# Kernel optimization log

Hardware: AMD Instinct MI355X
Metric: run time of the kernel (lower is better)

The kernel has to match this reference:

```python
import jax, jax.numpy as jnp
import numpy as np

T = 2_000_000  # seq_len
I, H, O = 2, 30, 1  # input_size, hidden_size, output_size


def setup_inputs() -> dict:
    key = jax.random.key(0)
    ks = jax.random.split(key, 7)
    s = 1.0 / np.sqrt(H)  # torch default uniform(-1/sqrt(H), 1/sqrt(H)) scale
    return {
        "x": jax.random.normal(ks[0], (T, I), dtype=jnp.float32),
        "W_ih": jax.random.uniform(ks[1], (H, I), jnp.float32, -s, s),
        "W_hh": jax.random.uniform(ks[2], (H, H), jnp.float32, -s, s),
        "b_ih": jax.random.uniform(ks[3], (H,), jnp.float32, -s, s),
        "b_hh": jax.random.uniform(ks[4], (H,), jnp.float32, -s, s),
        "W_fc": jax.random.uniform(ks[5], (O, H), jnp.float32, -s, s),
        "b_fc": jax.random.uniform(ks[6], (O,), jnp.float32, -s, s),
    }


def reference(x, W_ih, W_hh, b_ih, b_hh, W_fc, b_fc):
    # Elman RNN (torch.nn.RNN, tanh): h_t = tanh(x_t W_ih^T + b_ih + h_{t-1} W_hh^T + b_hh)
    # Precompute the input projection for all timesteps in one GEMM.
    xp = x @ W_ih.T + (b_ih + b_hh)  # [T, H]

    def step(h, xt):
        h = jnp.tanh(xt + h @ W_hh.T)
        return h, h

    h0 = jnp.zeros((H,), dtype=x.dtype)
    _, hs = jax.lax.scan(step, h0, xp)  # hs: [T, H]
    return hs @ W_fc.T + b_fc  # [T, O]
```

## Files before the change

kernel.cpp:

```cpp
#include <hip/hip_runtime.h>


#define T_LEN     2000000
#define HID       30
#define CHUNK_LEN 64
#define BURN      15
#define NBLOCK    512
#define WSTEPS    8
#define NWIN      10
#define NCHUNK_ST 31250

typedef __attribute__((ext_vector_type(8))) _Float16 half8;
typedef __attribute__((ext_vector_type(2))) __fp16   fp16x2;
typedef __attribute__((ext_vector_type(4))) float    float4v;

union h8u { half8 v8; fp16x2 v2[4]; unsigned u2[4]; };
union h2u { fp16x2 v; unsigned u; };

#define PREFETCH(O) {                                                        \
    _Pragma("unroll")                                                        \
    for (int s = 0; s < WSTEPS; ++s) {                                       \
        int tt = wbase + (O) * WSTEPS + s;                                   \
        tt = tt < 0 ? 0 : (tt >= T_LEN ? T_LEN - 1 : tt);                    \
        nxt[s] = xf2[tt];                                                    \
    }                                                                        \
}

#define CONVERT() {                                                          \
    _Pragma("unroll")                                                        \
    for (int s = 0; s < WSTEPS; ++s) {                                       \
        h2u c; c.v = __builtin_amdgcn_cvt_pkrtz(nxt[s].x, nxt[s].y);         \
        xcur[s] = c.u;                                                       \
    }                                                                        \
}

#define STEP_BODY(XC, S, MASKQ, STOREQ)                                      \
{                                                                            \
    float th[8];                                                             \
    _Pragma("unroll")                                                        \
    for (int i = 0; i < 4; ++i) {                                            \
        th[i]   = 1.f - 2.f * __builtin_amdgcn_rcpf(1.f + __builtin_amdgcn_exp2f(d_t[i])); \
        th[4+i] = 1.f - 2.f * __builtin_amdgcn_rcpf(1.f + __builtin_amdgcn_exp2f(d_b[i])); \
    }                                                                        \
    if (MASKQ) {                                                             \
        const float m = (t_cur >= 1) ? 1.f : 0.f;                            \
        _Pragma("unroll")                                                    \
        for (int i = 0; i < 8; ++i) th[i] *= m;                              \
    }                                                                        \
    h8u b;                                                                   \
    b.v2[0] = __builtin_amdgcn_cvt_pkrtz(th[0], th[1]);                      \
    b.v2[1] = __builtin_amdgcn_cvt_pkrtz(th[2], th[3]);                      \
    b.v2[2] = __builtin_amdgcn_cvt_pkrtz(th[4], th[5]);                      \
    b.v2[3] = __builtin_amdgcn_cvt_pkrtz(th[6], th[7]);                      \
    if (g3) b.u2[3] = (XC);                                                  \
    d_t = __builtin_amdgcn_mfma_f32_16x16x32_f16(a_t.v8, b.v8, cT, 0, 0, 0); \
    d_b = __builtin_amdgcn_mfma_f32_16x16x32_f16(a_b.v8, b.v8, cB, 0, 0, 0); \
    if (STOREQ) {                                                            \
        obuf[(S) & 3] = d_b[2];                                              \
        if (((S) & 3) == 3 && st_ok) {                                       \
            *(float4v*)(optr + (o - 2) * WSTEPS + (S) - 3) = obuf;           \
        }                                                                    \
    }                                                                        \
    ++t_cur;                                                                 \
}

__global__ __launch_bounds__(256, 2)
void rnn_mfma_kernel(const float* __restrict__ x,
                     const float* __restrict__ W_ih,
                     const float* __restrict__ W_hh,
                     const float* __restrict__ b_ih,
                     const float* __restrict__ b_hh,
                     const float* __restrict__ W_fc,
                     const float* __restrict__ b_fc,
                     float* __restrict__ out)
{
    const int tid  = threadIdx.x;
    const int wave = tid >> 6;
    const int lane = tid & 63;
    const int g    = lane >> 4;
    const int cl   = lane & 15;
    const bool g3  = (g == 3);

    const int chunk = blockIdx.x * 64 + wave * 16 + cl;
    const int wbase = chunk * CHUNK_LEN - BURN;
    const float2* __restrict__ xf2 = (const float2*)x;

    const float SC = 2.0f * 1.44269504088896340736f;

    h8u a_t, a_b;
#pragma unroll
    for (int i = 0; i < 4; ++i) {
        const int k0 = 4*g + i;
        const int k1 = 16 + 4*g + i;
        const int mt = cl;
        const int mb = 16 + cl;

        a_t.v8[i] = (_Float16)(SC * W_hh[mt*HID + k0]);
        float v_t1;
        if (k1 < HID)        v_t1 = SC * W_hh[mt*HID + k1];
        else if (k1 == HID)  v_t1 = SC * W_ih[mt*2 + 0];
        else                 v_t1 = SC * W_ih[mt*2 + 1];
        a_t.v8[4+i] = (_Float16)v_t1;

        float v_b0, v_b1;
        if (mb < HID) {
            v_b0 = SC * W_hh[mb*HID + k0];
            if (k1 < HID)        v_b1 = SC * W_hh[mb*HID + k1];
            else if (k1 == HID)  v_b1 = SC * W_ih[mb*2 + 0];
            else                 v_b1 = SC * W_ih[mb*2 + 1];
        } else if (mb == HID) {
            v_b0 = W_fc[k0];
            v_b1 = (k1 < HID) ? W_fc[k1] : 0.f;
        } else {
            v_b0 = 0.f; v_b1 = 0.f;
        }
        a_b.v8[i]   = (_Float16)v_b0;
        a_b.v8[4+i] = (_Float16)v_b1;
    }

    float4v cT, cB;
#pragma unroll
    for (int i = 0; i < 4; ++i) {
        const int rt  = 4*g + i;
        const int rb2 = 16 + 4*g + i;
        cT[i] = SC * (b_ih[rt] + b_hh[rt]);
        cB[i] = (rb2 < HID)  ? SC * (b_ih[rb2] + b_hh[rb2])
              : (rb2 == HID) ? b_fc[0] : 0.f;
    }

    const bool st_ok = g3 && (chunk < NCHUNK_ST);
    float* const optr = out + chunk * CHUNK_LEN;

    __builtin_amdgcn_sched_barrier(0);

    float4v d_t = {0.f,0.f,0.f,0.f}, d_b = {0.f,0.f,0.f,0.f};
    float4v obuf;

    int t_cur = wbase;

    float2   nxt[WSTEPS];
    unsigned xcur[WSTEPS];

    PREFETCH(0)

#pragma clang loop unroll(disable)
    for (int o = 0; o < 2; ++o) {
        CONVERT()
        PREFETCH(o + 1)
#pragma unroll
        for (int s = 0; s < WSTEPS; ++s) {
            STEP_BODY(xcur[s], s, true, false)
        }
    }

#pragma clang loop unroll(disable)
    for (int o = 2; o < NWIN; ++o) {
        CONVERT()
        if (o < NWIN - 1) { PREFETCH(o + 1) }
#pragma unroll
        for (int s = 0; s < WSTEPS; ++s) {
            STEP_BODY(xcur[s], s, false, true)
        }
    }
}

extern "C" void kernel_launch(void* const* d_in, const int* in_sizes, int n_in,
                              void* d_out, int out_size, void* d_ws, size_t ws_size,
                              hipStream_t stream)
{
    const float* x    = (const float*)d_in[0];
    const float* W_ih = (const float*)d_in[1];
    const float* W_hh = (const float*)d_in[2];
    const float* b_ih = (const float*)d_in[3];
    const float* b_hh = (const float*)d_in[4];
    const float* W_fc = (const float*)d_in[5];
    const float* b_fc = (const float*)d_in[6];
    float* out = (float*)d_out;

    rnn_mfma_kernel<<<NBLOCK, 256, 0, stream>>>(x, W_ih, W_hh, b_ih, b_hh,
                                                W_fc, b_fc, out);
}
```

Before: 99.37 us.

## Fold tanh affine terms into weights and share reciprocals across pairs

Rewrites tanh as 1 - 2*sigmoid-like term and moves the 1 - 2*(.) affine part into the MFMA weights and bias. The recurrent and output weights are prescaled by -2 and the bias is offset by a precomputed MFMA with a constant -0.5 vector. Each step then feeds 1/(1+e) directly, and one reciprocal is shared per pair via 1/(a0*a1), which halves the rcp count on the serial critical path. The risks are that a0*a1 can overflow for large pre-activations and that rounding differs under fp16.

After: 99.45 us. Within noise of the previous version (+0.1%).

```diff
diff --git a/kernel.cpp b/kernel.cpp
--- a/kernel.cpp
+++ b/kernel.cpp
@@ -36,22 +36,34 @@
 
 #define STEP_BODY(XC, S, MASKQ, STOREQ)                                      \
 {                                                                            \
-    float th[8];                                                             \
-    _Pragma("unroll")                                                        \
-    for (int i = 0; i < 4; ++i) {                                            \
-        th[i]   = 1.f - 2.f * __builtin_amdgcn_rcpf(1.f + __builtin_amdgcn_exp2f(d_t[i])); \
-        th[4+i] = 1.f - 2.f * __builtin_amdgcn_rcpf(1.f + __builtin_amdgcn_exp2f(d_b[i])); \
+    h8u b;                                                                   \
+    {                                                                        \
+        const float e0 = __builtin_amdgcn_exp2f(d_t[0]);                     \
+        const float e1 = __builtin_amdgcn_exp2f(d_t[1]);                     \
+        const float e2 = __builtin_amdgcn_exp2f(d_t[2]);                     \
+        const float e3 = __builtin_amdgcn_exp2f(d_t[3]);                     \
+        const float e4 = __builtin_amdgcn_exp2f(d_b[0]);                     \
+        const float e5 = __builtin_amdgcn_exp2f(d_b[1]);                     \
+        const float e6 = __builtin_amdgcn_exp2f(d_b[2]);                     \
+        const float e7 = __builtin_amdgcn_exp2f(d_b[3]);                     \
+        const float a0 = 1.f + e0, a1 = 1.f + e1, a2 = 1.f + e2,             \
+                    a3 = 1.f + e3, a4 = 1.f + e4, a5 = 1.f + e5,             \
+                    a6 = 1.f + e6, a7 = 1.f + e7;                            \
+        const float rP0 = __builtin_amdgcn_rcpf(a0 * a1);                    \
+        const float rP1 = __builtin_amdgcn_rcpf(a2 * a3);                    \
+        const float rP2 = __builtin_amdgcn_rcpf(a4 * a5);                    \
+        const float rP3 = __builtin_amdgcn_rcpf(a6 * a7);                    \
+        b.v2[0] = __builtin_amdgcn_cvt_pkrtz(a1 * rP0, a0 * rP0);            \
+        b.v2[1] = __builtin_amdgcn_cvt_pkrtz(a3 * rP1, a2 * rP1);            \
+        b.v2[2] = __builtin_amdgcn_cvt_pkrtz(a5 * rP2, a4 * rP2);            \
+        b.v2[3] = __builtin_amdgcn_cvt_pkrtz(a7 * rP3, a6 * rP3);            \
     }                                                                        \
     if (MASKQ) {                                                             \
-        const float m = (t_cur >= 1) ? 1.f : 0.f;                            \
-        _Pragma("unroll")                                                    \
-        for (int i = 0; i < 8; ++i) th[i] *= m;                              \
-    }                                                                        \
-    h8u b;                                                                   \
-    b.v2[0] = __builtin_amdgcn_cvt_pkrtz(th[0], th[1]);                      \
-    b.v2[1] = __builtin_amdgcn_cvt_pkrtz(th[2], th[3]);                      \
-    b.v2[2] = __builtin_amdgcn_cvt_pkrtz(th[4], th[5]);                      \
-    b.v2[3] = __builtin_amdgcn_cvt_pkrtz(th[6], th[7]);                      \
+        if (t_cur < 1) {                                                     \
+            b.u2[0] = 0x38003800u; b.u2[1] = 0x38003800u;                    \
+            b.u2[2] = 0x38003800u; b.u2[3] = 0x38003800u;                    \
+        }                                                                    \
+    }                                                                        \
     if (g3) b.u2[3] = (XC);                                                  \
     d_t = __builtin_amdgcn_mfma_f32_16x16x32_f16(a_t.v8, b.v8, cT, 0, 0, 0); \
     d_b = __builtin_amdgcn_mfma_f32_16x16x32_f16(a_b.v8, b.v8, cB, 0, 0, 0); \
@@ -86,6 +98,7 @@
     const float2* __restrict__ xf2 = (const float2*)x;
 
     const float SC = 2.0f * 1.44269504088896340736f;
+    const float FS = -2.0f * SC;
 
     h8u a_t, a_b;
 #pragma unroll
@@ -95,22 +108,22 @@
         const int mt = cl;
         const int mb = 16 + cl;
 
-        a_t.v8[i] = (_Float16)(SC * W_hh[mt*HID + k0]);
+        a_t.v8[i] = (_Float16)(FS * W_hh[mt*HID + k0]);
         float v_t1;
-        if (k1 < HID)        v_t1 = SC * W_hh[mt*HID + k1];
+        if (k1 < HID)        v_t1 = FS * W_hh[mt*HID + k1];
         else if (k1 == HID)  v_t1 = SC * W_ih[mt*2 + 0];
         else                 v_t1 = SC * W_ih[mt*2 + 1];
         a_t.v8[4+i] = (_Float16)v_t1;
 
         float v_b0, v_b1;
         if (mb < HID) {
-            v_b0 = SC * W_hh[mb*HID + k0];
-            if (k1 < HID)        v_b1 = SC * W_hh[mb*HID + k1];
+            v_b0 = FS * W_hh[mb*HID + k0];
+            if (k1 < HID)        v_b1 = FS * W_hh[mb*HID + k1];
             else if (k1 == HID)  v_b1 = SC * W_ih[mb*2 + 0];
             else                 v_b1 = SC * W_ih[mb*2 + 1];
         } else if (mb == HID) {
-            v_b0 = W_fc[k0];
-            v_b1 = (k1 < HID) ? W_fc[k1] : 0.f;
+            v_b0 = -2.f * W_fc[k0];
+            v_b1 = (k1 < HID) ? -2.f * W_fc[k1] : 0.f;
         } else {
             v_b0 = 0.f; v_b1 = 0.f;
         }
@@ -126,6 +139,15 @@
         cT[i] = SC * (b_ih[rt] + b_hh[rt]);
         cB[i] = (rb2 < HID)  ? SC * (b_ih[rb2] + b_hh[rb2])
               : (rb2 == HID) ? b_fc[0] : 0.f;
+    }
+
+    {
+        h8u bh;
+        bh.u2[0] = 0xB800B800u; bh.u2[1] = 0xB800B800u;
+        bh.u2[2] = 0xB800B800u; bh.u2[3] = 0xB800B800u;
+        if (g3) bh.u2[3] = 0u;
+        cT = __builtin_amdgcn_mfma_f32_16x16x32_f16(a_t.v8, bh.v8, cT, 0, 0, 0);
+        cB = __builtin_amdgcn_mfma_f32_16x16x32_f16(a_b.v8, bh.v8, cB, 0, 0, 0);
     }
 
     const bool st_ok = g3 && (chunk < NCHUNK_ST);
```
